# Performance work log

Measured on AMD Instinct MI355X. Metric: run time of the kernel, lower is better.

## Reference

```python
import jax, jax.numpy as jnp
import numpy as np

D = H = W = 128
NUM_STEPS = 7  # MONAI DVF2DDF default


def _base_grid(dtype):
    zz, yy, xx = jnp.meshgrid(jnp.arange(D, dtype=dtype),
                              jnp.arange(H, dtype=dtype),
                              jnp.arange(W, dtype=dtype), indexing='ij')
    return jnp.stack([zz, yy, xx], 0)  # [3,D,H,W] voxel coords


def _warp(img, ddf, mode):
    # img: [1,C,D,H,W], ddf: [1,3,D,H,W] in voxel units.
    # Equivalent to grid_sample(align_corners=True, padding='border'):
    # border padding == clamp the voxel-space sample coordinate to [0, dim-1].
    dtype = ddf.dtype
    coords = _base_grid(dtype) + ddf[0]
    lims = jnp.array([D - 1, H - 1, W - 1], dtype=dtype).reshape(3, 1, 1, 1)
    coords = jnp.clip(coords, 0.0, lims)
    vol = img[0]  # [C,D,H,W]
    if mode == 'nearest':
        zi, yi, xi = jnp.round(coords).astype(jnp.int32)
        return vol[:, zi, yi, xi][None]
    z, y, x = coords
    z0 = jnp.floor(z); y0 = jnp.floor(y); x0 = jnp.floor(x)
    wz = z - z0; wy = y - y0; wx = x - x0
    z0i = z0.astype(jnp.int32); y0i = y0.astype(jnp.int32); x0i = x0.astype(jnp.int32)
    z1i = jnp.minimum(z0i + 1, D - 1)
    y1i = jnp.minimum(y0i + 1, H - 1)
    x1i = jnp.minimum(x0i + 1, W - 1)
    g = lambda a, b, c: vol[:, a, b, c]  # [C,D,H,W] gather
    out = (g(z0i, y0i, x0i) * (1 - wz) * (1 - wy) * (1 - wx)
         + g(z0i, y0i, x1i) * (1 - wz) * (1 - wy) * wx
         + g(z0i, y1i, x0i) * (1 - wz) * wy * (1 - wx)
         + g(z0i, y1i, x1i) * (1 - wz) * wy * wx
         + g(z1i, y0i, x0i) * wz * (1 - wy) * (1 - wx)
         + g(z1i, y0i, x1i) * wz * (1 - wy) * wx
         + g(z1i, y1i, x0i) * wz * wy * (1 - wx)
         + g(z1i, y1i, x1i) * wz * wy * wx)
    return out[None]


def _dvf2ddf(dvf):
    # scaling-and-squaring integration of a stationary velocity field
    ddf = dvf / (2.0 ** NUM_STEPS)
    for _ in range(NUM_STEPS):
        ddf = ddf + _warp(ddf, ddf, 'bilinear')
    return ddf


def setup_inputs() -> dict:
    key = jax.random.key(0)
    k1, k2, k3, k4 = jax.random.split(key, 4)
    dvf = jax.random.normal(k1, (1, 3, D, H, W), dtype=jnp.float32) * 0.5
    moving_image = jax.random.uniform(k2, (1, 1, D, H, W), dtype=jnp.float32)
    fixed_image = jax.random.uniform(k3, (1, 1, D, H, W), dtype=jnp.float32)
    moving_label = jax.random.randint(k4, (1, 1, D, H, W), 0, 4).astype(jnp.float32)
    return {'dvf': dvf, 'moving_image': moving_image,
            'fixed_image': fixed_image, 'moving_label': moving_label}


def reference(dvf, moving_image, fixed_image, moving_label):
    ddf = _dvf2ddf(dvf)
    pred_image = _warp(moving_image, ddf, 'bilinear')
    pred_label = _warp(moving_label, ddf, 'nearest')
    return (ddf, pred_image, pred_label, dvf)
```

## Files before the change

### kernel.cpp

```cpp
#include <hip/hip_runtime.h>

#define DD 128
constexpr int NV = DD * DD * DD;
constexpr float INV_SCALE = 1.0f / 128.0f;

__device__ __forceinline__ void unpack_zyx(int tid, int& z, int& y, int& x) {
    x = tid & (DD - 1);
    y = (tid >> 7) & (DD - 1);
    z = tid >> 14;
}

__device__ __forceinline__ float clamp01(float v) {
    return fminf(fmaxf(v, 0.0f), (float)(DD - 1));
}

__global__ __launch_bounds__(256)
void init_kernel(const float* __restrict__ dvf, float* __restrict__ A) {
    int tid = blockIdx.x * blockDim.x + threadIdx.x;
    float d0 = dvf[tid] * INV_SCALE;
    float d1 = dvf[tid + NV] * INV_SCALE;
    float d2 = dvf[tid + 2 * NV] * INV_SCALE;
    float* p = A + 3 * tid;
    p[0] = d0; p[1] = d1; p[2] = d2;
}

__device__ __forceinline__ void trilerp3(const float* __restrict__ src,
                                         float cz, float cy, float cx,
                                         float& r0, float& r1, float& r2) {
    float z0f = floorf(cz), y0f = floorf(cy), x0f = floorf(cx);
    float wz = cz - z0f, wy = cy - y0f, wx = cx - x0f;
    int z0 = (int)z0f, y0 = (int)y0f, x0 = (int)x0f;
    int z1 = min(z0 + 1, DD - 1);
    int y1 = min(y0 + 1, DD - 1);
    int x1 = min(x0 + 1, DD - 1);
    float omz = 1.0f - wz, omy = 1.0f - wy, omx = 1.0f - wx;

    int zs0 = z0 << 14, zs1 = z1 << 14;
    int ys0 = y0 << 7,  ys1 = y1 << 7;

    const float* p000 = src + 3 * (zs0 + ys0 + x0);
    const float* p001 = src + 3 * (zs0 + ys0 + x1);
    const float* p010 = src + 3 * (zs0 + ys1 + x0);
    const float* p011 = src + 3 * (zs0 + ys1 + x1);
    const float* p100 = src + 3 * (zs1 + ys0 + x0);
    const float* p101 = src + 3 * (zs1 + ys0 + x1);
    const float* p110 = src + 3 * (zs1 + ys1 + x0);
    const float* p111 = src + 3 * (zs1 + ys1 + x1);

    float w000 = omz * omy * omx, w001 = omz * omy * wx;
    float w010 = omz * wy * omx,  w011 = omz * wy * wx;
    float w100 = wz * omy * omx,  w101 = wz * omy * wx;
    float w110 = wz * wy * omx,   w111 = wz * wy * wx;

    r0 = w000 * p000[0] + w001 * p001[0] + w010 * p010[0] + w011 * p011[0]
       + w100 * p100[0] + w101 * p101[0] + w110 * p110[0] + w111 * p111[0];
    r1 = w000 * p000[1] + w001 * p001[1] + w010 * p010[1] + w011 * p011[1]
       + w100 * p100[1] + w101 * p101[1] + w110 * p110[1] + w111 * p111[1];
    r2 = w000 * p000[2] + w001 * p001[2] + w010 * p010[2] + w011 * p011[2]
       + w100 * p100[2] + w101 * p101[2] + w110 * p110[2] + w111 * p111[2];
}

template <bool PLANAR_OUT>
__global__ __launch_bounds__(256)
void step_kernel(const float* __restrict__ src, float* __restrict__ dst) {
    int tid = blockIdx.x * blockDim.x + threadIdx.x;
    int z, y, x;
    unpack_zyx(tid, z, y, x);

    const float* s = src + 3 * tid;
    float d0 = s[0], d1 = s[1], d2 = s[2];

    float cz = clamp01((float)z + d0);
    float cy = clamp01((float)y + d1);
    float cx = clamp01((float)x + d2);

    float r0, r1, r2;
    trilerp3(src, cz, cy, cx, r0, r1, r2);

    r0 += d0; r1 += d1; r2 += d2;

    if (PLANAR_OUT) {
        dst[tid]          = r0;
        dst[tid + NV]     = r1;
        dst[tid + 2 * NV] = r2;
    } else {
        float* p = dst + 3 * tid;
        p[0] = r0; p[1] = r1; p[2] = r2;
    }
}

__global__ __launch_bounds__(256)
void final_kernel(const float* __restrict__ ddf,
                  const float* __restrict__ mimg,
                  const float* __restrict__ mlab,
                  const float* __restrict__ dvf,
                  float* __restrict__ pred_img,
                  float* __restrict__ pred_lab,
                  float* __restrict__ dvf_out) {
    int tid = blockIdx.x * blockDim.x + threadIdx.x;
    int z, y, x;
    unpack_zyx(tid, z, y, x);

    float d0 = ddf[tid];
    float d1 = ddf[tid + NV];
    float d2 = ddf[tid + 2 * NV];

    float cz = clamp01((float)z + d0);
    float cy = clamp01((float)y + d1);
    float cx = clamp01((float)x + d2);

    {
        float z0f = floorf(cz), y0f = floorf(cy), x0f = floorf(cx);
        float wz = cz - z0f, wy = cy - y0f, wx = cx - x0f;
        int z0 = (int)z0f, y0 = (int)y0f, x0 = (int)x0f;
        int z1 = min(z0 + 1, DD - 1);
        int y1 = min(y0 + 1, DD - 1);
        int x1 = min(x0 + 1, DD - 1);
        float omz = 1.0f - wz, omy = 1.0f - wy, omx = 1.0f - wx;
        int zs0 = z0 << 14, zs1 = z1 << 14;
        int ys0 = y0 << 7,  ys1 = y1 << 7;

        float v = omz * omy * omx * mimg[zs0 + ys0 + x0]
                + omz * omy * wx  * mimg[zs0 + ys0 + x1]
                + omz * wy * omx  * mimg[zs0 + ys1 + x0]
                + omz * wy * wx   * mimg[zs0 + ys1 + x1]
                + wz * omy * omx  * mimg[zs1 + ys0 + x0]
                + wz * omy * wx   * mimg[zs1 + ys0 + x1]
                + wz * wy * omx   * mimg[zs1 + ys1 + x0]
                + wz * wy * wx    * mimg[zs1 + ys1 + x1];
        pred_img[tid] = v;
    }

    {
        int zi = (int)rintf(cz);
        int yi = (int)rintf(cy);
        int xi = (int)rintf(cx);
        pred_lab[tid] = mlab[(zi << 14) + (yi << 7) + xi];
    }

    dvf_out[tid]          = dvf[tid];
    dvf_out[tid + NV]     = dvf[tid + NV];
    dvf_out[tid + 2 * NV] = dvf[tid + 2 * NV];
}

extern "C" void kernel_launch(void* const* d_in, const int* in_sizes, int n_in,
                              void* d_out, int out_size, void* d_ws, size_t ws_size,
                              hipStream_t stream) {
    const float* dvf  = (const float*)d_in[0];
    const float* mimg = (const float*)d_in[1];
    const float* mlab = (const float*)d_in[3];

    float* out      = (float*)d_out;
    float* ddf_out  = out;
    float* pred_img = out + 3 * NV;
    float* pred_lab = out + 4 * NV;
    float* dvf_out  = out + 5 * NV;

    float* A = dvf_out;
    float* B = ddf_out;

    dim3 block(256);
    dim3 grid(NV / 256);

    init_kernel<<<grid, block, 0, stream>>>(dvf, A);
    step_kernel<false><<<grid, block, 0, stream>>>(A, B);
    step_kernel<false><<<grid, block, 0, stream>>>(B, A);
    step_kernel<false><<<grid, block, 0, stream>>>(A, B);
    step_kernel<false><<<grid, block, 0, stream>>>(B, A);
    step_kernel<false><<<grid, block, 0, stream>>>(A, B);
    step_kernel<false><<<grid, block, 0, stream>>>(B, A);
    step_kernel<true ><<<grid, block, 0, stream>>>(A, B);
    final_kernel<<<grid, block, 0, stream>>>(B, mimg, mlab, dvf,
                                             pred_img, pred_lab, dvf_out);
}
```

Baseline: 260.2 us.

## Fuse init into first step, fuse last step with final warp, swizzle block order

```diff
diff --git a/kernel.cpp b/kernel.cpp
--- a/kernel.cpp
+++ b/kernel.cpp
@@ -2,7 +2,11 @@
 
 #define DD 128
 constexpr int NV = DD * DD * DD;
-constexpr float INV_SCALE = 1.0f / 128.0f;
+constexpr float SCALE = 1.0f / 128.0f;
+
+__device__ __forceinline__ int swizzle_block(int b) {
+    return (b & 7) * 1024 + (b >> 3);
+}
 
 __device__ __forceinline__ void unpack_zyx(int tid, int& z, int& y, int& x) {
     x = tid & (DD - 1);
@@ -10,23 +14,16 @@
     z = tid >> 14;
 }
 
-__device__ __forceinline__ float clamp01(float v) {
+__device__ __forceinline__ float clampc(float v) {
     return fminf(fmaxf(v, 0.0f), (float)(DD - 1));
 }
 
-__global__ __launch_bounds__(256)
-void init_kernel(const float* __restrict__ dvf, float* __restrict__ A) {
-    int tid = blockIdx.x * blockDim.x + threadIdx.x;
-    float d0 = dvf[tid] * INV_SCALE;
-    float d1 = dvf[tid + NV] * INV_SCALE;
-    float d2 = dvf[tid + 2 * NV] * INV_SCALE;
-    float* p = A + 3 * tid;
-    p[0] = d0; p[1] = d1; p[2] = d2;
-}
+struct Corners {
+    int i000, i001, i010, i011, i100, i101, i110, i111;
+    float w000, w001, w010, w011, w100, w101, w110, w111;
+};
 
-__device__ __forceinline__ void trilerp3(const float* __restrict__ src,
-                                         float cz, float cy, float cx,
-                                         float& r0, float& r1, float& r2) {
+__device__ __forceinline__ Corners corner_setup(float cz, float cy, float cx) {
     float z0f = floorf(cz), y0f = floorf(cy), x0f = floorf(cx);
     float wz = cz - z0f, wy = cy - y0f, wx = cx - x0f;
     int z0 = (int)z0f, y0 = (int)y0f, x0 = (int)x0f;
@@ -34,113 +31,139 @@
     int y1 = min(y0 + 1, DD - 1);
     int x1 = min(x0 + 1, DD - 1);
     float omz = 1.0f - wz, omy = 1.0f - wy, omx = 1.0f - wx;
-
     int zs0 = z0 << 14, zs1 = z1 << 14;
     int ys0 = y0 << 7,  ys1 = y1 << 7;
-
-    const float* p000 = src + 3 * (zs0 + ys0 + x0);
-    const float* p001 = src + 3 * (zs0 + ys0 + x1);
-    const float* p010 = src + 3 * (zs0 + ys1 + x0);
-    const float* p011 = src + 3 * (zs0 + ys1 + x1);
-    const float* p100 = src + 3 * (zs1 + ys0 + x0);
-    const float* p101 = src + 3 * (zs1 + ys0 + x1);
-    const float* p110 = src + 3 * (zs1 + ys1 + x0);
-    const float* p111 = src + 3 * (zs1 + ys1 + x1);
-
-    float w000 = omz * omy * omx, w001 = omz * omy * wx;
-    float w010 = omz * wy * omx,  w011 = omz * wy * wx;
-    float w100 = wz * omy * omx,  w101 = wz * omy * wx;
-    float w110 = wz * wy * omx,   w111 = wz * wy * wx;
-
-    r0 = w000 * p000[0] + w001 * p001[0] + w010 * p010[0] + w011 * p011[0]
-       + w100 * p100[0] + w101 * p101[0] + w110 * p110[0] + w111 * p111[0];
-    r1 = w000 * p000[1] + w001 * p001[1] + w010 * p010[1] + w011 * p011[1]
-       + w100 * p100[1] + w101 * p101[1] + w110 * p110[1] + w111 * p111[1];
-    r2 = w000 * p000[2] + w001 * p001[2] + w010 * p010[2] + w011 * p011[2]
-       + w100 * p100[2] + w101 * p101[2] + w110 * p110[2] + w111 * p111[2];
+    Corners c;
+    c.i000 = zs0 + ys0 + x0; c.i001 = zs0 + ys0 + x1;
+    c.i010 = zs0 + ys1 + x0; c.i011 = zs0 + ys1 + x1;
+    c.i100 = zs1 + ys0 + x0; c.i101 = zs1 + ys0 + x1;
+    c.i110 = zs1 + ys1 + x0; c.i111 = zs1 + ys1 + x1;
+    c.w000 = omz * omy * omx; c.w001 = omz * omy * wx;
+    c.w010 = omz * wy * omx;  c.w011 = omz * wy * wx;
+    c.w100 = wz * omy * omx;  c.w101 = wz * omy * wx;
+    c.w110 = wz * wy * omx;   c.w111 = wz * wy * wx;
+    return c;
 }
 
-template <bool PLANAR_OUT>
+__device__ __forceinline__ void trilerp3i(const float* __restrict__ src,
+                                          const Corners& c,
+                                          float& r0, float& r1, float& r2) {
+    const float* p000 = src + 3 * c.i000; const float* p001 = src + 3 * c.i001;
+    const float* p010 = src + 3 * c.i010; const float* p011 = src + 3 * c.i011;
+    const float* p100 = src + 3 * c.i100; const float* p101 = src + 3 * c.i101;
+    const float* p110 = src + 3 * c.i110; const float* p111 = src + 3 * c.i111;
+    r0 = c.w000*p000[0] + c.w001*p001[0] + c.w010*p010[0] + c.w011*p011[0]
+       + c.w100*p100[0] + c.w101*p101[0] + c.w110*p110[0] + c.w111*p111[0];
+    r1 = c.w000*p000[1] + c.w001*p001[1] + c.w010*p010[1] + c.w011*p011[1]
+       + c.w100*p100[1] + c.w101*p101[1] + c.w110*p110[1] + c.w111*p111[1];
+    r2 = c.w000*p000[2] + c.w001*p001[2] + c.w010*p010[2] + c.w011*p011[2]
+       + c.w100*p100[2] + c.w101*p101[2] + c.w110*p110[2] + c.w111*p111[2];
+}
+
+__global__ __launch_bounds__(256)
+void step1_kernel(const float* __restrict__ dvf, float* __restrict__ dst) {
+    int b = swizzle_block(blockIdx.x);
+    int tid = b * 256 + threadIdx.x;
+    int z, y, x;
+    unpack_zyx(tid, z, y, x);
+
+    float d0 = dvf[tid] * SCALE;
+    float d1 = dvf[tid + NV] * SCALE;
+    float d2 = dvf[tid + 2 * NV] * SCALE;
+
+    Corners c = corner_setup(clampc((float)z + d0),
+                             clampc((float)y + d1),
+                             clampc((float)x + d2));
+
+    float r0 = 0.f, r1 = 0.f, r2 = 0.f;
+    {
+        const float* s0 = dvf;
+        const float* s1 = dvf + NV;
+        const float* s2 = dvf + 2 * NV;
+        r0 = c.w000*s0[c.i000] + c.w001*s0[c.i001] + c.w010*s0[c.i010] + c.w011*s0[c.i011]
+           + c.w100*s0[c.i100] + c.w101*s0[c.i101] + c.w110*s0[c.i110] + c.w111*s0[c.i111];
+        r1 = c.w000*s1[c.i000] + c.w001*s1[c.i001] + c.w010*s1[c.i010] + c.w011*s1[c.i011]
+           + c.w100*s1[c.i100] + c.w101*s1[c.i101] + c.w110*s1[c.i110] + c.w111*s1[c.i111];
+        r2 = c.w000*s2[c.i000] + c.w001*s2[c.i001] + c.w010*s2[c.i010] + c.w011*s2[c.i011]
+           + c.w100*s2[c.i100] + c.w101*s2[c.i101] + c.w110*s2[c.i110] + c.w111*s2[c.i111];
+    }
+
+    float* p = dst + 3 * tid;
+    p[0] = d0 + r0 * SCALE;
+    p[1] = d1 + r1 * SCALE;
+    p[2] = d2 + r2 * SCALE;
+}
+
 __global__ __launch_bounds__(256)
 void step_kernel(const float* __restrict__ src, float* __restrict__ dst) {
-    int tid = blockIdx.x * blockDim.x + threadIdx.x;
+    int b = swizzle_block(blockIdx.x);
+    int tid = b * 256 + threadIdx.x;
     int z, y, x;
     unpack_zyx(tid, z, y, x);
 
     const float* s = src + 3 * tid;
     float d0 = s[0], d1 = s[1], d2 = s[2];
 
-    float cz = clamp01((float)z + d0);
-    float cy = clamp01((float)y + d1);
-    float cx = clamp01((float)x + d2);
+    Corners c = corner_setup(clampc((float)z + d0),
+                             clampc((float)y + d1),
+                             clampc((float)x + d2));
+    float r0, r1, r2;
+    trilerp3i(src, c, r0, r1, r2);
 
-    float r0, r1, r2;
-    trilerp3(src, cz, cy, cx, r0, r1, r2);
-
-    r0 += d0; r1 += d1; r2 += d2;
-
-    if (PLANAR_OUT) {
-        dst[tid]          = r0;
-        dst[tid + NV]     = r1;
-        dst[tid + 2 * NV] = r2;
-    } else {
-        float* p = dst + 3 * tid;
-        p[0] = r0; p[1] = r1; p[2] = r2;
-    }
+    float* p = dst + 3 * tid;
+    p[0] = d0 + r0; p[1] = d1 + r1; p[2] = d2 + r2;
 }
 
 __global__ __launch_bounds__(256)
-void final_kernel(const float* __restrict__ ddf,
-                  const float* __restrict__ mimg,
-                  const float* __restrict__ mlab,
-                  const float* __restrict__ dvf,
-                  float* __restrict__ pred_img,
-                  float* __restrict__ pred_lab,
-                  float* __restrict__ dvf_out) {
-    int tid = blockIdx.x * blockDim.x + threadIdx.x;
+void step7_final_kernel(const float* __restrict__ src,
+                        const float* __restrict__ mimg,
+                        const float* __restrict__ mlab,
+                        float* __restrict__ ddf_out,
+                        float* __restrict__ pred_img,
+                        float* __restrict__ pred_lab) {
+    int b = swizzle_block(blockIdx.x);
+    int tid = b * 256 + threadIdx.x;
     int z, y, x;
     unpack_zyx(tid, z, y, x);
 
-    float d0 = ddf[tid];
-    float d1 = ddf[tid + NV];
-    float d2 = ddf[tid + 2 * NV];
+    const float* s = src + 3 * tid;
+    float d0 = s[0], d1 = s[1], d2 = s[2];
 
-    float cz = clamp01((float)z + d0);
-    float cy = clamp01((float)y + d1);
-    float cx = clamp01((float)x + d2);
+    Corners c = corner_setup(clampc((float)z + d0),
+                             clampc((float)y + d1),
+                             clampc((float)x + d2));
+    float r0, r1, r2;
+    trilerp3i(src, c, r0, r1, r2);
+
+    r0 += d0; r1 += d1; r2 += d2;
+    ddf_out[tid]          = r0;
+    ddf_out[tid + NV]     = r1;
+    ddf_out[tid + 2 * NV] = r2;
+
+    float cz = clampc((float)z + r0);
+    float cy = clampc((float)y + r1);
+    float cx = clampc((float)x + r2);
 
     {
-        float z0f = floorf(cz), y0f = floorf(cy), x0f = floorf(cx);
-        float wz = cz - z0f, wy = cy - y0f, wx = cx - x0f;
-        int z0 = (int)z0f, y0 = (int)y0f, x0 = (int)x0f;
-        int z1 = min(z0 + 1, DD - 1);
-        int y1 = min(y0 + 1, DD - 1);
-        int x1 = min(x0 + 1, DD - 1);
-        float omz = 1.0f - wz, omy = 1.0f - wy, omx = 1.0f - wx;
-        int zs0 = z0 << 14, zs1 = z1 << 14;
-        int ys0 = y0 << 7,  ys1 = y1 << 7;
-
-        float v = omz * omy * omx * mimg[zs0 + ys0 + x0]
-                + omz * omy * wx  * mimg[zs0 + ys0 + x1]
-                + omz * wy * omx  * mimg[zs0 + ys1 + x0]
-                + omz * wy * wx   * mimg[zs0 + ys1 + x1]
-                + wz * omy * omx  * mimg[zs1 + ys0 + x0]
-                + wz * omy * wx   * mimg[zs1 + ys0 + x1]
-                + wz * wy * omx   * mimg[zs1 + ys1 + x0]
-                + wz * wy * wx    * mimg[zs1 + ys1 + x1];
+        Corners g = corner_setup(cz, cy, cx);
+        float v = g.w000*mimg[g.i000] + g.w001*mimg[g.i001]
+                + g.w010*mimg[g.i010] + g.w011*mimg[g.i011]
+                + g.w100*mimg[g.i100] + g.w101*mimg[g.i101]
+                + g.w110*mimg[g.i110] + g.w111*mimg[g.i111];
         pred_img[tid] = v;
     }
-
     {
         int zi = (int)rintf(cz);
         int yi = (int)rintf(cy);
         int xi = (int)rintf(cx);
         pred_lab[tid] = mlab[(zi << 14) + (yi << 7) + xi];
     }
+}
 
-    dvf_out[tid]          = dvf[tid];
-    dvf_out[tid + NV]     = dvf[tid + NV];
-    dvf_out[tid + 2 * NV] = dvf[tid + 2 * NV];
+__global__ __launch_bounds__(256)
+void copy_dvf_kernel(const float4* __restrict__ dvf, float4* __restrict__ dvf_out) {
+    int tid = blockIdx.x * blockDim.x + threadIdx.x;
+    dvf_out[tid] = dvf[tid];
 }
 
 extern "C" void kernel_launch(void* const* d_in, const int* in_sizes, int n_in,
@@ -162,14 +185,14 @@
     dim3 block(256);
     dim3 grid(NV / 256);
 
-    init_kernel<<<grid, block, 0, stream>>>(dvf, A);
-    step_kernel<false><<<grid, block, 0, stream>>>(A, B);
-    step_kernel<false><<<grid, block, 0, stream>>>(B, A);
-    step_kernel<false><<<grid, block, 0, stream>>>(A, B);
-    step_kernel<false><<<grid, block, 0, stream>>>(B, A);
-    step_kernel<false><<<grid, block, 0, stream>>>(A, B);
-    step_kernel<false><<<grid, block, 0, stream>>>(B, A);
-    step_kernel<true ><<<grid, block, 0, stream>>>(A, B);
-    final_kernel<<<grid, block, 0, stream>>>(B, mimg, mlab, dvf,
-                                             pred_img, pred_lab, dvf_out);
+    step1_kernel<<<grid, block, 0, stream>>>(dvf, B);
+    step_kernel<<<grid, block, 0, stream>>>(B, A);
+    step_kernel<<<grid, block, 0, stream>>>(A, B);
+    step_kernel<<<grid, block, 0, stream>>>(B, A);
+    step_kernel<<<grid, block, 0, stream>>>(A, B);
+    step_kernel<<<grid, block, 0, stream>>>(B, A);
+    step7_final_kernel<<<grid, block, 0, stream>>>(A, mimg, mlab,
+                                                   ddf_out, pred_img, pred_lab);
+    copy_dvf_kernel<<<3 * NV / (4 * 256), block, 0, stream>>>(
+        (const float4*)dvf, (float4*)dvf_out);
 }
```

After: 267.8 us. 2.9% more time.
